# Kernel tuning notes

Hardware: AMD Instinct MI355X
Metric: run time of the kernel (lower is better)

Reference implementation:

```python
import jax, jax.numpy as jnp
import numpy as np

B, S, D = 512, 512, 768
VOCAB = 30522
CLS, SEP, PAD = 101, 102, 0


def setup_inputs() -> dict:
    key = jax.random.key(0)
    k1, k2 = jax.random.split(key)
    embed = jax.random.normal(k1, (B, S, D), dtype=jnp.float32)
    token_ids = jax.random.randint(k2, (B, S), 0, VOCAB, dtype=jnp.int64)
    return {"embed": embed, "token_ids": token_ids}


def reference(embed, token_ids):
    # mask out [CLS]=101, [SEP]=102, [PAD]=0; mean over remaining tokens
    mask = (token_ids != CLS) & (token_ids != SEP) & (token_ids != PAD)  # [B, S]
    maskf = mask.astype(embed.dtype)
    summed = jnp.einsum('bsd,bs->bd', embed, maskf)           # [B, D]
    count = jnp.sum(maskf, axis=-1, keepdims=True)            # [B, 1]
    return summed / count
```

## Files before the change

### kernel.cpp

```cpp
#include <hip/hip_runtime.h>


constexpr int B = 512;
constexpr int S = 512;
constexpr int D = 768;
constexpr int NV = D / 4;

__global__ __launch_bounds__(NV) void masked_mean_kernel(
    const float4* __restrict__ embed,
    const int* __restrict__ tok,
    float4* __restrict__ out)
{
    const int b = blockIdx.x;
    const int t = threadIdx.x;

    __shared__ float maskf[S];

    for (int s = t; s < S; s += NV) {
        int id = tok[b * S + s];
        maskf[s] = (id != 0 && id != 101 && id != 102) ? 1.0f : 0.0f;
    }
    __syncthreads();

    const float4* row = embed + (size_t)b * S * NV + t;
    float4 acc = make_float4(0.f, 0.f, 0.f, 0.f);
    float cnt = 0.f;

#pragma unroll 8
    for (int s = 0; s < S; ++s) {
        const float m = maskf[s];
        const float4 v = row[(size_t)s * NV];
        cnt += m;
        acc.x = fmaf(v.x, m, acc.x);
        acc.y = fmaf(v.y, m, acc.y);
        acc.z = fmaf(v.z, m, acc.z);
        acc.w = fmaf(v.w, m, acc.w);
    }

    const float inv = 1.0f / cnt;
    out[b * NV + t] = make_float4(acc.x * inv, acc.y * inv, acc.z * inv, acc.w * inv);
}

extern "C" void kernel_launch(void* const* d_in, const int* in_sizes, int n_in,
                              void* d_out, int out_size, void* d_ws, size_t ws_size,
                              hipStream_t stream) {
    const float4* embed = (const float4*)d_in[0];
    const int* tok = (const int*)d_in[1];
    float4* out = (float4*)d_out;

    masked_mean_kernel<<<dim3(B), dim3(NV), 0, stream>>>(embed, tok, out);
}
```

Before: 996.1 us.

## Split sequence reduction across blocks with partial sums and a finalize kernel

Splits the per-batch reduction over the sequence into 8 chunks, each handled by a separate block that writes partial sums and counts to workspace. A second kernel combines the partials and divides by the count. The aim is far more blocks and in-flight memory requests to saturate HBM bandwidth, at the cost of an extra launch and a small partial-sum round trip.

```diff
diff --git a/kernel.cpp b/kernel.cpp
--- a/kernel.cpp
+++ b/kernel.cpp
@@ -5,31 +5,35 @@
 constexpr int S = 512;
 constexpr int D = 768;
 constexpr int NV = D / 4;
+constexpr int SPLIT = 8;
+constexpr int SCHUNK = S / SPLIT;
 
-__global__ __launch_bounds__(NV) void masked_mean_kernel(
+__global__ __launch_bounds__(NV) void partial_kernel(
     const float4* __restrict__ embed,
     const int* __restrict__ tok,
-    float4* __restrict__ out)
+    float4* __restrict__ psum,
+    float* __restrict__ pcnt)
 {
     const int b = blockIdx.x;
+    const int p = blockIdx.y;
     const int t = threadIdx.x;
+    const int s0 = p * SCHUNK;
 
-    __shared__ float maskf[S];
-
-    for (int s = t; s < S; s += NV) {
-        int id = tok[b * S + s];
-        maskf[s] = (id != 0 && id != 101 && id != 102) ? 1.0f : 0.0f;
+    __shared__ float maskf[SCHUNK];
+    if (t < SCHUNK) {
+        int id = tok[b * S + s0 + t];
+        maskf[t] = (id != 0 && id != 101 && id != 102) ? 1.0f : 0.0f;
     }
     __syncthreads();
 
-    const float4* row = embed + (size_t)b * S * NV + t;
+    const float4* row = embed + ((size_t)b * S + s0) * NV + t;
     float4 acc = make_float4(0.f, 0.f, 0.f, 0.f);
     float cnt = 0.f;
 
 #pragma unroll 8
-    for (int s = 0; s < S; ++s) {
-        const float m = maskf[s];
-        const float4 v = row[(size_t)s * NV];
+    for (int i = 0; i < SCHUNK; ++i) {
+        const float m = maskf[i];
+        const float4 v = row[(size_t)i * NV];
         cnt += m;
         acc.x = fmaf(v.x, m, acc.x);
         acc.y = fmaf(v.y, m, acc.y);
@@ -37,6 +41,26 @@
         acc.w = fmaf(v.w, m, acc.w);
     }
 
+    psum[((size_t)b * SPLIT + p) * NV + t] = acc;
+    if (t == 0) pcnt[b * SPLIT + p] = cnt;
+}
+
+__global__ __launch_bounds__(NV) void finalize_kernel(
+    const float4* __restrict__ psum,
+    const float* __restrict__ pcnt,
+    float4* __restrict__ out)
+{
+    const int b = blockIdx.x;
+    const int t = threadIdx.x;
+
+    float4 acc = make_float4(0.f, 0.f, 0.f, 0.f);
+    float cnt = 0.f;
+#pragma unroll
+    for (int p = 0; p < SPLIT; ++p) {
+        const float4 v = psum[((size_t)b * SPLIT + p) * NV + t];
+        acc.x += v.x; acc.y += v.y; acc.z += v.z; acc.w += v.w;
+        cnt += pcnt[b * SPLIT + p];
+    }
     const float inv = 1.0f / cnt;
     out[b * NV + t] = make_float4(acc.x * inv, acc.y * inv, acc.z * inv, acc.w * inv);
 }
@@ -48,5 +72,9 @@
     const int* tok = (const int*)d_in[1];
     float4* out = (float4*)d_out;
 
-    masked_mean_kernel<<<dim3(B), dim3(NV), 0, stream>>>(embed, tok, out);
+    float4* psum = (float4*)d_ws;
+    float* pcnt = (float*)((char*)d_ws + (size_t)B * SPLIT * NV * sizeof(float4));
+
+    partial_kernel<<<dim3(B, SPLIT), dim3(NV), 0, stream>>>(embed, tok, psum, pcnt);
+    finalize_kernel<<<dim3(B), dim3(NV), 0, stream>>>(psum, pcnt, out);
 }
```

New measurement: 1.011 ms. Within noise of the previous version (+1.5%).
